# Performance work log

Hardware: AMD Instinct MI355X
Metric: run time of the kernel (lower is better)

The kernel has to match this reference:

```python
import jax, jax.numpy as jnp
import numpy as np
from jax import lax

B, L, D = 2, 2048, 2048
H, DK, DV, K = 16, 128, 128, 4
Q_DIM = H * DK  # 2048
V_DIM = H * DV  # 2048


def setup_inputs() -> dict:
    key = jax.random.key(0)
    ks = jax.random.split(key, 16)
    s = 0.02
    f32 = jnp.float32
    return {
        "hidden_states": jax.random.normal(ks[0], (B, L, D), f32),
        "Wq": jax.random.normal(ks[1], (D, Q_DIM), f32) * s,
        "Wk": jax.random.normal(ks[2], (D, Q_DIM), f32) * s,
        "Wv": jax.random.normal(ks[3], (D, V_DIM), f32) * s,
        "Wb": jax.random.normal(ks[4], (D, H), f32) * s,
        "bb": jnp.full((H,), -2.0, f32),  # beta_proj bias init -2.0
        "Wg": jax.random.normal(ks[5], (D, V_DIM), f32) * s,
        "Wo": jax.random.normal(ks[6], (V_DIM, D), f32) * s,
        "qconv_w": jax.random.normal(ks[7], (Q_DIM, K), f32) * 0.5,
        "qconv_b": jnp.zeros((Q_DIM,), f32),
        "kconv_w": jax.random.normal(ks[8], (Q_DIM, K), f32) * 0.5,
        "kconv_b": jnp.zeros((Q_DIM,), f32),
        "qn_w": jnp.ones((DK,), f32),
        "qn_b": jnp.zeros((DK,), f32),
        "kn_w": jnp.ones((DK,), f32),
        "kn_b": jnp.zeros((DK,), f32),
    }


def silu(x):
    return x * jax.nn.sigmoid(x)


def causal_dwconv(x, w, b):
    # x: (B,L,C), depthwise causal conv, w: (C,K), b: (C,)
    Kk = w.shape[1]
    xp = jnp.pad(x, ((0, 0), (Kk - 1, 0), (0, 0)))
    kern = w.T[:, None, :]  # (K, 1, C) for WIO depthwise
    y = lax.conv_general_dilated(
        xp, kern, window_strides=(1,), padding='VALID',
        dimension_numbers=('NWC', 'WIO', 'NWC'),
        feature_group_count=w.shape[0])
    return y + b


def layernorm(x, w, b, eps=1e-5):
    m = jnp.mean(x, axis=-1, keepdims=True)
    var = jnp.mean((x - m) ** 2, axis=-1, keepdims=True)
    return (x - m) * lax.rsqrt(var + eps) * w + b


def reference(hidden_states, Wq, Wk, Wv, Wb, bb, Wg, Wo,
              qconv_w, qconv_b, kconv_w, kconv_b, qn_w, qn_b, kn_w, kn_b):
    Bs, Ls, Ds = hidden_states.shape
    q = hidden_states @ Wq
    k = hidden_states @ Wk
    v = hidden_states @ Wv
    beta = jax.nn.sigmoid(hidden_states @ Wb + bb)        # (B,L,H)
    gate = silu(hidden_states @ Wg)                       # (B,L,V)
    q = silu(causal_dwconv(q, qconv_w, qconv_b))
    k = silu(causal_dwconv(k, kconv_w, kconv_b))
    q = layernorm(q.reshape(Bs, Ls, H, DK), qn_w, qn_b)
    k = layernorm(k.reshape(Bs, Ls, H, DK), kn_w, kn_b)
    v = v.reshape(Bs, Ls, H, DV)
    # time-major for scan: (L,B,H,*)
    qs = q.transpose(1, 0, 2, 3)
    ks_ = k.transpose(1, 0, 2, 3)
    vs = v.transpose(1, 0, 2, 3)
    bs = beta.transpose(1, 0, 2)                          # (L,B,H)
    S0 = jnp.zeros((Bs, H, DV, DK), hidden_states.dtype)

    def step(S, inp):
        q_t, k_t, v_t, b_t = inp
        b = b_t[..., None, None]                          # (B,H,1,1)
        S = (1.0 - b) * S + b * (v_t[..., :, None] * k_t[..., None, :])
        o_t = jnp.einsum('bhvk,bhk->bhv', S, q_t)
        return S, o_t

    _, os = lax.scan(step, S0, (qs, ks_, vs, bs))         # os: (L,B,H,DV)
    o = os.transpose(1, 0, 2, 3).reshape(Bs, Ls, H * DV)
    o = o * gate
    return o @ Wo
```

## Files before the change

kernel.cpp:

```cpp
#include <hip/hip_runtime.h>

#define DEV __device__ __forceinline__

typedef __attribute__((ext_vector_type(4))) float f32x4;
typedef __attribute__((ext_vector_type(8))) short s16x8;
typedef __attribute__((ext_vector_type(8))) unsigned short u16x8;
typedef __attribute__((ext_vector_type(4))) unsigned short u16x4;

DEV unsigned short f2bf(float f) {
    union { float f; unsigned u; } v; v.f = f;
    unsigned r = v.u + 0x7fffu + ((v.u >> 16) & 1u);
    return (unsigned short)(r >> 16);
}
DEV float bf2f(unsigned short b) {
    union { unsigned u; float f; } v; v.u = ((unsigned)b) << 16;
    return v.f;
}
DEV f32x4 mfma16(s16x8 a, s16x8 b, f32x4 c) {
    return __builtin_amdgcn_mfma_f32_16x16x32_bf16(a, b, c, 0, 0, 0);
}
DEV float sigmoidf_(float x) { return 1.f / (1.f + __expf(-x)); }

typedef __attribute__((address_space(3))) unsigned int lds_u32;
typedef const __attribute__((address_space(1))) unsigned int glob_u32;
DEV void gload16(const void* g, void* l) {
    __builtin_amdgcn_global_load_lds((glob_u32*)g, (lds_u32*)l, 16, 0, 0);
}

static constexpr int Bc = 2, Lc = 2048, Dc = 2048, Hc = 16, DKc = 128;

__global__ __launch_bounds__(256) void hsconv_kernel(const float* __restrict__ src,
                                                     unsigned short* __restrict__ dst) {
    size_t i8 = ((size_t)blockIdx.x * 256 + threadIdx.x) * 8;
    f32x4 a = *(const f32x4*)(src + i8);
    f32x4 b = *(const f32x4*)(src + i8 + 4);
    u16x8 r;
    for (int j = 0; j < 4; ++j) { r[j] = f2bf(a[j]); r[j + 4] = f2bf(b[j]); }
    *(u16x8*)(dst + i8) = r;
}

struct WcArgs { const float* src[5]; unsigned short* dst[5]; };

__global__ __launch_bounds__(256) void wconv_kernel(WcArgs wa) {
    __shared__ unsigned short t[64][66];
    const float* __restrict__ src = wa.src[blockIdx.z];
    unsigned short* __restrict__ dst = wa.dst[blockIdx.z];
    const int k0 = blockIdx.x * 64, n0 = blockIdx.y * 64;
    const int tid = threadIdx.x;
    for (int it = 0; it < 4; ++it) {
        int idx = it * 256 + tid;
        int k = idx >> 4, n = (idx & 15) * 4;
        f32x4 v = *(const f32x4*)(src + (size_t)(k0 + k) * 2048 + n0 + n);
        for (int j = 0; j < 4; ++j) t[k][n + j] = f2bf(v[j]);
    }
    __syncthreads();
    for (int it = 0; it < 4; ++it) {
        int idx = it * 256 + tid;
        int n = idx >> 4, k = (idx & 15) * 4;
        u16x4 o;
        for (int j = 0; j < 4; ++j) o[j] = t[k + j][n];
        *(u16x4*)(dst + (size_t)(n0 + n) * 2048 + k0 + k) = o;
    }
}

__global__ __launch_bounds__(256) void wbt_kernel(const float* __restrict__ Wb,
                                                  unsigned short* __restrict__ wbt) {
    int g = blockIdx.x * 256 + threadIdx.x;
    int n = g >> 8;
    int k0 = (g & 255) * 8;
    u16x8 r;
    for (int j = 0; j < 8; ++j) r[j] = f2bf(Wb[(size_t)(k0 + j) * 16 + n]);
    *(u16x8*)(wbt + (size_t)n * 2048 + k0) = r;
}

struct GpArgs { const unsigned short* B[4]; unsigned short* C[4]; };

#define GEMM_BODY(A_, Bt_, KDIM)                                                          \
    __shared__ unsigned short As[128 * 64];                                               \
    __shared__ unsigned short Bs[128 * 64];                                               \
    const int tid = threadIdx.x, lane = tid & 63, wid = tid >> 6;                         \
    const int l15 = lane & 15, lq = lane >> 4;                                            \
    const int wr = wid >> 1, wc = wid & 1;                                                \
    const int m0 = blockIdx.x * 128, n0 = blockIdx.y * 128;                               \
    const int rsub = lane >> 3, csub = (lane & 7) * 8;                                    \
    f32x4 acc[4][4] = {};                                                                 \
    for (int kt = 0; kt < KDIM; kt += 64) {                                               \
        for (int j = 0; j < 4; ++j) {                                                     \
            int seg = j * 4 + wid;                                                        \
            gload16(A_ + (size_t)(m0 + seg * 8 + rsub) * KDIM + kt + csub, &As[seg * 512]); \
            gload16(Bt_ + (size_t)(n0 + seg * 8 + rsub) * KDIM + kt + csub, &Bs[seg * 512]); \
        }                                                                                 \
        __syncthreads();                                                                  \
        for (int kh = 0; kh < 2; ++kh) {                                                  \
            s16x8 af[4];                                                                  \
            for (int m16 = 0; m16 < 4; ++m16)                                             \
                af[m16] = *(const s16x8*)&As[(wr * 64 + m16 * 16 + l15) * 64 + kh * 32 + 8 * lq]; \
            for (int n16 = 0; n16 < 4; ++n16) {                                           \
                s16x8 bf = *(const s16x8*)&Bs[(wc * 64 + n16 * 16 + l15) * 64 + kh * 32 + 8 * lq]; \
                for (int m16 = 0; m16 < 4; ++m16)                                         \
                    acc[m16][n16] = mfma16(af[m16], bf, acc[m16][n16]);                   \
            }                                                                             \
        }                                                                                 \
        __syncthreads();                                                                  \
    }

__global__ __launch_bounds__(256) void gemm_proj(const unsigned short* __restrict__ A,
                                                 GpArgs ga, int N, int K) {
    const unsigned short* __restrict__ Bt = ga.B[blockIdx.z];
    GEMM_BODY(A, Bt, K)
    unsigned short* __restrict__ C = ga.C[blockIdx.z];
    for (int m16 = 0; m16 < 4; ++m16)
        for (int n16 = 0; n16 < 4; ++n16) {
            int row = m0 + wr * 64 + m16 * 16 + 4 * lq;
            int col = n0 + wc * 64 + n16 * 16 + l15;
            for (int j = 0; j < 4; ++j)
                C[(size_t)(row + j) * N + col] = f2bf(acc[m16][n16][j]);
        }
}

__global__ __launch_bounds__(256) void gemm_out(const unsigned short* __restrict__ A,
                                                const unsigned short* __restrict__ Bt,
                                                float* __restrict__ C, int N, int K) {
    GEMM_BODY(A, Bt, K)
    for (int m16 = 0; m16 < 4; ++m16)
        for (int n16 = 0; n16 < 4; ++n16) {
            int row = m0 + wr * 64 + m16 * 16 + 4 * lq;
            int col = n0 + wc * 64 + n16 * 16 + l15;
            for (int j = 0; j < 4; ++j)
                C[(size_t)(row + j) * N + col] = acc[m16][n16][j];
        }
}

__global__ __launch_bounds__(256) void beta_kernel(const unsigned short* __restrict__ hsb,
                                                   const unsigned short* __restrict__ wbt,
                                                   const float* __restrict__ bb,
                                                   float* __restrict__ bbuf,
                                                   float* __restrict__ labuf) {
    const int tid = threadIdx.x, lane = tid & 63, wid = tid >> 6;
    const int l15 = lane & 15, lq = lane >> 4;
    const int row16 = blockIdx.x * 64 + wid * 16;
    f32x4 acc = {};
    for (int kt = 0; kt < 2048; kt += 32) {
        s16x8 a = *(const s16x8*)(hsb + (size_t)(row16 + l15) * 2048 + kt + 8 * lq);
        s16x8 b = *(const s16x8*)(wbt + (size_t)l15 * 2048 + kt + 8 * lq);
        acc = mfma16(a, b, acc);
    }
    float bias = bb[l15];
    for (int j = 0; j < 4; ++j) {
        int i = row16 + 4 * lq + j;
        float x = acc[j] + bias;
        bbuf[(size_t)i * 16 + l15] = sigmoidf_(x);
        labuf[(size_t)i * 16 + l15] = -(fmaxf(x, 0.f) + log1pf(__expf(-fabsf(x))));
    }
}

__global__ __launch_bounds__(256) void convln_kernel(const unsigned short* __restrict__ src,
                                                     const float* __restrict__ cw,
                                                     const float* __restrict__ cb,
                                                     const float* __restrict__ lw,
                                                     const float* __restrict__ lb,
                                                     unsigned short* __restrict__ dst) {
    const int bl = blockIdx.x;
    const int tid = threadIdx.x;
    const int b = bl >> 11, l = bl & 2047;
    const int c0 = tid * 8;
    const int ch0 = c0 & 127;
    f32x4 wv[8];
    for (int i = 0; i < 8; ++i) wv[i] = *(const f32x4*)(cw + (size_t)(c0 + i) * 4);
    float acc[8];
    {
        f32x4 ca = *(const f32x4*)(cb + c0);
        f32x4 cbv = *(const f32x4*)(cb + c0 + 4);
        for (int i = 0; i < 4; ++i) { acc[i] = ca[i]; acc[4 + i] = cbv[i]; }
    }
    for (int j = 0; j < 4; ++j) {
        int lj = l - 3 + j;
        if (lj < 0) continue;
        u16x8 v = *(const u16x8*)(src + ((size_t)(b * 2048 + lj)) * 2048 + c0);
        for (int i = 0; i < 8; ++i) acc[i] += wv[i][j] * bf2f(v[i]);
    }
    float y[8];
    float s1 = 0.f, s2 = 0.f;
    for (int i = 0; i < 8; ++i) {
        float t = acc[i];
        t = t * sigmoidf_(t);
        y[i] = t; s1 += t; s2 += t * t;
    }
    for (int o = 8; o; o >>= 1) { s1 += __shfl_xor(s1, o, 16); s2 += __shfl_xor(s2, o, 16); }
    float m = s1 * (1.f / 128.f);
    float var = s2 * (1.f / 128.f) - m * m;
    float r = rsqrtf(var + 1e-5f);
    f32x4 lwa = *(const f32x4*)(lw + ch0), lwb = *(const f32x4*)(lw + ch0 + 4);
    f32x4 lba = *(const f32x4*)(lb + ch0), lbb = *(const f32x4*)(lb + ch0 + 4);
    u16x8 outv;
    for (int i = 0; i < 4; ++i) {
        outv[i]     = f2bf((y[i]     - m) * r * lwa[i] + lba[i]);
        outv[4 + i] = f2bf((y[4 + i] - m) * r * lwb[i] + lbb[i]);
    }
    *(u16x8*)(dst + (size_t)bl * 2048 + c0) = outv;
}

__global__ __launch_bounds__(256) void recur_kernel(const unsigned short* __restrict__ qln,
                                                    const unsigned short* __restrict__ kln,
                                                    const unsigned short* __restrict__ vp,
                                                    const float* __restrict__ bbuf,
                                                    const float* __restrict__ labuf,
                                                    unsigned short* __restrict__ orec) {
    __shared__ unsigned short Qs[64][136];
    __shared__ unsigned short Ks[64][136];
    __shared__ unsigned short Kt[128][72];
    __shared__ unsigned short Vt[32][72];
    __shared__ unsigned short Ps[64][72];
    __shared__ unsigned short Simg[32][136];
    __shared__ float ls[64], es[64], wsc[64], bsc[64];
    __shared__ float gam;

    const int tid = threadIdx.x;
    const int lane = tid & 63, wid = tid >> 6;
    const int l15 = lane & 15, lq = lane >> 4;
    const int bh = blockIdx.x, vs = blockIdx.y;
    const int b = bh >> 4, h = bh & 15;
    const size_t rowBase = (size_t)b * 2048;
    const int voff = h * 128 + vs * 32;
    const int vt_own = wid & 1;
    const int ktb = (wid >> 1) * 4;

    f32x4 accS[4] = {};

    for (int ch = 0; ch < 32; ++ch) {
        const int t0 = ch * 64;
        if (wid == 0) {
            float la = labuf[(rowBase + t0 + lane) * 16 + h];
            float bv = bbuf[(rowBase + t0 + lane) * 16 + h];
            float l = la;
            for (int o = 1; o < 64; o <<= 1) { float n = __shfl_up(l, o, 64); if (lane >= o) l += n; }
            ls[lane] = l;
            es[lane] = __expf(l);
            float l63 = __shfl(l, 63, 64);
            wsc[lane] = __expf(l63 - l) * bv;
            bsc[lane] = bv;
            if (lane == 0) gam = __expf(l63);
            for (int it = 0; it < 16; ++it) {
                int idx = it * 64 + lane;
                int r = idx >> 4, c8 = (idx & 15) * 8;
                *(u16x8*)&Qs[r][c8] = *(const u16x8*)(qln + (rowBase + t0 + r) * 2048 + h * 128 + c8);
            }
        } else if (wid == 1) {
            for (int it = 0; it < 16; ++it) {
                int idx = it * 64 + lane;
                int r = idx >> 4, c8 = (idx & 15) * 8;
                *(u16x8*)&Ks[r][c8] = *(const u16x8*)(kln + (rowBase + t0 + r) * 2048 + h * 128 + c8);
            }
        } else if (wid == 2) {
            for (int c8 = 0; c8 < 128; c8 += 8) {
                u16x8 kv = *(const u16x8*)(kln + (rowBase + t0 + lane) * 2048 + h * 128 + c8);
                for (int ii = 0; ii < 8; ++ii) Kt[c8 + ii][lane] = kv[ii];
            }
        } else {
            for (int c8 = 0; c8 < 32; c8 += 8) {
                u16x8 vv = *(const u16x8*)(vp + (rowBase + t0 + lane) * 2048 + voff + c8);
                for (int ii = 0; ii < 8; ++ii) Vt[c8 + ii][lane] = vv[ii];
            }
        }
        __syncthreads();

        {
            const int i0 = wid * 16;
            f32x4 accp[4] = {};
            for (int kt = 0; kt < 4; ++kt) {
                s16x8 af = *(const s16x8*)&Qs[i0 + l15][kt * 32 + 8 * lq];
                for (int s16i = 0; s16i < 4; ++s16i) {
                    s16x8 bf = *(const s16x8*)&Ks[s16i * 16 + l15][kt * 32 + 8 * lq];
                    accp[s16i] = mfma16(af, bf, accp[s16i]);
                }
            }
            for (int s16i = 0; s16i < 4; ++s16i)
                for (int j = 0; j < 4; ++j) {
                    int i = i0 + 4 * lq + j;
                    int s = s16i * 16 + l15;
                    float pv = accp[s16i][j];
                    pv = (s <= i) ? pv * __expf(ls[i] - ls[s]) * bsc[s] : 0.f;
                    Ps[i][s] = f2bf(pv);
                }
            for (int q = 0; q < 4; ++q)
                for (int j = 0; j < 4; ++j) {
                    int v = vt_own * 16 + 4 * lq + j;
                    int k = (ktb + q) * 16 + l15;
                    Simg[v][k] = f2bf(accS[q][j]);
                }
        }
        __syncthreads();

        {
            const int i0 = wid * 16;
            f32x4 ae[2] = {}, ai[2] = {};
            for (int kt = 0; kt < 4; ++kt) {
                s16x8 af = *(const s16x8*)&Qs[i0 + l15][kt * 32 + 8 * lq];
                for (int vt = 0; vt < 2; ++vt) {
                    s16x8 bf = *(const s16x8*)&Simg[vt * 16 + l15][kt * 32 + 8 * lq];
                    ae[vt] = mfma16(af, bf, ae[vt]);
                }
            }
            for (int st = 0; st < 2; ++st) {
                s16x8 af = *(const s16x8*)&Ps[i0 + l15][st * 32 + 8 * lq];
                for (int vt = 0; vt < 2; ++vt) {
                    s16x8 bf = *(const s16x8*)&Vt[vt * 16 + l15][st * 32 + 8 * lq];
                    ai[vt] = mfma16(af, bf, ai[vt]);
                }
            }
            for (int vt = 0; vt < 2; ++vt)
                for (int j = 0; j < 4; ++j) {
                    int i = i0 + 4 * lq + j;
                    float o = es[i] * ae[vt][j] + ai[vt][j];
                    orec[(rowBase + t0 + i) * 2048 + voff + vt * 16 + l15] = f2bf(o);
                }
        }

        {
            float g = gam;
            for (int q = 0; q < 4; ++q)
                for (int j = 0; j < 4; ++j) accS[q][j] *= g;
            for (int st = 0; st < 2; ++st) {
                s16x8 vraw = *(const s16x8*)&Vt[vt_own * 16 + l15][st * 32 + 8 * lq];
                s16x8 aw;
                for (int ii = 0; ii < 8; ++ii) {
                    int s = st * 32 + 8 * lq + ii;
                    aw[ii] = (short)f2bf(bf2f((unsigned short)vraw[ii]) * wsc[s]);
                }
                for (int q = 0; q < 4; ++q) {
                    s16x8 bf = *(const s16x8*)&Kt[(ktb + q) * 16 + l15][st * 32 + 8 * lq];
                    accS[q] = mfma16(aw, bf, accS[q]);
                }
            }
        }
        __syncthreads();
    }
}

__global__ __launch_bounds__(256) void gate_kernel(const unsigned short* __restrict__ o,
                                                   unsigned short* __restrict__ g) {
    size_t i8 = ((size_t)blockIdx.x * 256 + threadIdx.x) * 8;
    u16x8 ov = *(const u16x8*)(o + i8);
    u16x8 gv = *(const u16x8*)(g + i8);
    u16x8 r;
    for (int ii = 0; ii < 8; ++ii) {
        float gf = bf2f(gv[ii]);
        r[ii] = f2bf(bf2f(ov[ii]) * gf * sigmoidf_(gf));
    }
    *(u16x8*)(g + i8) = r;
}

extern "C" void kernel_launch(void* const* d_in, const int* in_sizes, int n_in,
                              void* d_out, int out_size, void* d_ws, size_t ws_size,
                              hipStream_t stream) {
    const float* hs  = (const float*)d_in[0];
    const float* Wq  = (const float*)d_in[1];
    const float* Wk  = (const float*)d_in[2];
    const float* Wv  = (const float*)d_in[3];
    const float* Wb  = (const float*)d_in[4];
    const float* bbv = (const float*)d_in[5];
    const float* Wg  = (const float*)d_in[6];
    const float* Wo  = (const float*)d_in[7];
    const float* qcw = (const float*)d_in[8];
    const float* qcb = (const float*)d_in[9];
    const float* kcw = (const float*)d_in[10];
    const float* kcb = (const float*)d_in[11];
    const float* qnw = (const float*)d_in[12];
    const float* qnb = (const float*)d_in[13];
    const float* knw = (const float*)d_in[14];
    const float* knb = (const float*)d_in[15];
    float* out = (float*)d_out;

    char* ws = (char*)d_ws;
    const size_t S2 = (size_t)Bc * Lc * 2048 * 2;
    const size_t WSb = (size_t)2048 * 2048 * 2;
    const size_t BB = (size_t)Bc * Lc * Hc * 4;
    unsigned short* hsb  = (unsigned short*)(ws);
    unsigned short* wqt  = (unsigned short*)(ws + S2);
    unsigned short* wkt  = (unsigned short*)(ws + S2 + 1 * WSb);
    unsigned short* wvt  = (unsigned short*)(ws + S2 + 2 * WSb);
    unsigned short* wgt  = (unsigned short*)(ws + S2 + 3 * WSb);
    unsigned short* wot  = (unsigned short*)(ws + S2 + 4 * WSb);
    unsigned short* qp   = (unsigned short*)(ws + S2 + 5 * WSb);
    unsigned short* kp   = (unsigned short*)(ws + S2 + 5 * WSb + 1 * S2);
    unsigned short* vp   = (unsigned short*)(ws + S2 + 5 * WSb + 2 * S2);
    unsigned short* gp   = (unsigned short*)(ws + S2 + 5 * WSb + 3 * S2);
    float* bbuf  = (float*)(ws + S2 + 5 * WSb + 4 * S2);
    float* labuf = (float*)(ws + S2 + 5 * WSb + 4 * S2 + BB);
    unsigned short* wbt = (unsigned short*)(ws + S2 + 5 * WSb + 4 * S2 + 2 * BB);
    unsigned short* qln  = wqt;
    unsigned short* kln  = wvt;
    unsigned short* orec = qp;

    const int M = Bc * Lc;

    hsconv_kernel<<<dim3(M * 2048 / (256 * 8)), dim3(256), 0, stream>>>(hs, hsb);
    WcArgs wa;
    wa.src[0] = Wq; wa.src[1] = Wk; wa.src[2] = Wv; wa.src[3] = Wg; wa.src[4] = Wo;
    wa.dst[0] = wqt; wa.dst[1] = wkt; wa.dst[2] = wvt; wa.dst[3] = wgt; wa.dst[4] = wot;
    wconv_kernel<<<dim3(32, 32, 5), dim3(256), 0, stream>>>(wa);
    wbt_kernel<<<dim3(16), dim3(256), 0, stream>>>(Wb, wbt);

    GpArgs ga;
    ga.B[0] = wqt; ga.B[1] = wkt; ga.B[2] = wvt; ga.B[3] = wgt;
    ga.C[0] = qp;  ga.C[1] = kp;  ga.C[2] = vp;  ga.C[3] = gp;
    gemm_proj<<<dim3(M / 128, 2048 / 128, 4), dim3(256), 0, stream>>>(hsb, ga, 2048, 2048);

    beta_kernel<<<dim3(M / 64), dim3(256), 0, stream>>>(hsb, wbt, bbv, bbuf, labuf);
    convln_kernel<<<dim3(M), dim3(256), 0, stream>>>(qp, qcw, qcb, qnw, qnb, qln);
    convln_kernel<<<dim3(M), dim3(256), 0, stream>>>(kp, kcw, kcb, knw, knb, kln);
    recur_kernel<<<dim3(Bc * Hc, 4), dim3(256), 0, stream>>>(qln, kln, vp, bbuf, labuf, orec);
    gate_kernel<<<dim3(M * 2048 / 8 / 256), dim3(256), 0, stream>>>(orec, gp);
    gemm_out<<<dim3(M / 128, 2048 / 128, 1), dim3(256), 0, stream>>>(gp, wot, out, 2048, 2048);
}
```

Before: 572.5 us.

## Split chunked recurrence into parallel local, state-scan, and cross-chunk kernels

Replaces the sequential per-(b,h) chunk loop, which ran on only 128 blocks, with three kernels. The first computes intra-chunk outputs and per-chunk state deltas for all 32 chunks in parallel. The second runs a cheap elementwise scan of the chunk states with the decay factors. The third adds the inter-chunk contribution Q·S to the outputs. This exposes far more parallelism on a large GPU, at the cost of writing chunk states to global memory in bf16 (reusing the hsb/kp buffers), extra launches, and a read-modify-write of orec.

```diff
diff --git a/kernel.cpp b/kernel.cpp
--- a/kernel.cpp
+++ b/kernel.cpp
@@ -28,6 +28,12 @@
 }
 
 static constexpr int Bc = 2, Lc = 2048, Dc = 2048, Hc = 16, DKc = 128;
+static constexpr size_t SLOT = 524288;
+
+DEV unsigned short* dslot(unsigned short* d0, unsigned short* d1, int c, int bh) {
+    unsigned short* p = (c < 16) ? d0 + (size_t)c * SLOT : d1 + (size_t)(c - 16) * SLOT;
+    return p + (size_t)bh * 16384;
+}
 
 __global__ __launch_bounds__(256) void hsconv_kernel(const float* __restrict__ src,
                                                      unsigned short* __restrict__ dst) {
@@ -200,140 +206,196 @@
     *(u16x8*)(dst + (size_t)bl * 2048 + c0) = outv;
 }
 
-__global__ __launch_bounds__(256) void recur_kernel(const unsigned short* __restrict__ qln,
-                                                    const unsigned short* __restrict__ kln,
-                                                    const unsigned short* __restrict__ vp,
-                                                    const float* __restrict__ bbuf,
-                                                    const float* __restrict__ labuf,
-                                                    unsigned short* __restrict__ orec) {
+__global__ __launch_bounds__(256) void recur_local(const unsigned short* __restrict__ qln,
+                                                   const unsigned short* __restrict__ kln,
+                                                   const unsigned short* __restrict__ vp,
+                                                   const float* __restrict__ bbuf,
+                                                   const float* __restrict__ labuf,
+                                                   unsigned short* __restrict__ orec,
+                                                   unsigned short* __restrict__ d0,
+                                                   unsigned short* __restrict__ d1,
+                                                   float* __restrict__ es_buf,
+                                                   float* __restrict__ gamma_buf) {
     __shared__ unsigned short Qs[64][136];
     __shared__ unsigned short Ks[64][136];
     __shared__ unsigned short Kt[128][72];
-    __shared__ unsigned short Vt[32][72];
+    __shared__ unsigned short Vt[128][72];
     __shared__ unsigned short Ps[64][72];
-    __shared__ unsigned short Simg[32][136];
-    __shared__ float ls[64], es[64], wsc[64], bsc[64];
-    __shared__ float gam;
+    __shared__ float ls[64], wsc[64], bsc[64];
 
     const int tid = threadIdx.x;
     const int lane = tid & 63, wid = tid >> 6;
     const int l15 = lane & 15, lq = lane >> 4;
-    const int bh = blockIdx.x, vs = blockIdx.y;
+    const int bh = blockIdx.x, c = blockIdx.y;
     const int b = bh >> 4, h = bh & 15;
     const size_t rowBase = (size_t)b * 2048;
-    const int voff = h * 128 + vs * 32;
-    const int vt_own = wid & 1;
-    const int ktb = (wid >> 1) * 4;
-
-    f32x4 accS[4] = {};
-
-    for (int ch = 0; ch < 32; ++ch) {
-        const int t0 = ch * 64;
-        if (wid == 0) {
-            float la = labuf[(rowBase + t0 + lane) * 16 + h];
-            float bv = bbuf[(rowBase + t0 + lane) * 16 + h];
-            float l = la;
-            for (int o = 1; o < 64; o <<= 1) { float n = __shfl_up(l, o, 64); if (lane >= o) l += n; }
-            ls[lane] = l;
-            es[lane] = __expf(l);
-            float l63 = __shfl(l, 63, 64);
-            wsc[lane] = __expf(l63 - l) * bv;
-            bsc[lane] = bv;
-            if (lane == 0) gam = __expf(l63);
-            for (int it = 0; it < 16; ++it) {
-                int idx = it * 64 + lane;
-                int r = idx >> 4, c8 = (idx & 15) * 8;
-                *(u16x8*)&Qs[r][c8] = *(const u16x8*)(qln + (rowBase + t0 + r) * 2048 + h * 128 + c8);
+    const int t0 = c * 64;
+
+    if (wid == 0) {
+        float la = labuf[(rowBase + t0 + lane) * 16 + h];
+        float bv = bbuf[(rowBase + t0 + lane) * 16 + h];
+        float l = la;
+        for (int o = 1; o < 64; o <<= 1) { float n = __shfl_up(l, o, 64); if (lane >= o) l += n; }
+        ls[lane] = l;
+        es_buf[(size_t)bh * 2048 + t0 + lane] = __expf(l);
+        float l63 = __shfl(l, 63, 64);
+        wsc[lane] = __expf(l63 - l) * bv;
+        bsc[lane] = bv;
+        if (lane == 0) gamma_buf[bh * 32 + c] = __expf(l63);
+        for (int it = 0; it < 16; ++it) {
+            int idx = it * 64 + lane;
+            int r = idx >> 4, c8 = (idx & 15) * 8;
+            *(u16x8*)&Qs[r][c8] = *(const u16x8*)(qln + (rowBase + t0 + r) * 2048 + h * 128 + c8);
+        }
+    } else if (wid == 1) {
+        for (int it = 0; it < 16; ++it) {
+            int idx = it * 64 + lane;
+            int r = idx >> 4, c8 = (idx & 15) * 8;
+            *(u16x8*)&Ks[r][c8] = *(const u16x8*)(kln + (rowBase + t0 + r) * 2048 + h * 128 + c8);
+        }
+    } else if (wid == 2) {
+        for (int c8 = 0; c8 < 128; c8 += 8) {
+            u16x8 kv = *(const u16x8*)(kln + (rowBase + t0 + lane) * 2048 + h * 128 + c8);
+            for (int ii = 0; ii < 8; ++ii) Kt[c8 + ii][lane] = kv[ii];
+        }
+    } else {
+        for (int c8 = 0; c8 < 128; c8 += 8) {
+            u16x8 vv = *(const u16x8*)(vp + (rowBase + t0 + lane) * 2048 + h * 128 + c8);
+            for (int ii = 0; ii < 8; ++ii) Vt[c8 + ii][lane] = vv[ii];
+        }
+    }
+    __syncthreads();
+
+    const int i0 = wid * 16;
+    {
+        f32x4 accp[4] = {};
+        for (int kt = 0; kt < 4; ++kt) {
+            s16x8 af = *(const s16x8*)&Qs[i0 + l15][kt * 32 + 8 * lq];
+            for (int s16i = 0; s16i < 4; ++s16i) {
+                s16x8 bf = *(const s16x8*)&Ks[s16i * 16 + l15][kt * 32 + 8 * lq];
+                accp[s16i] = mfma16(af, bf, accp[s16i]);
             }
-        } else if (wid == 1) {
-            for (int it = 0; it < 16; ++it) {
-                int idx = it * 64 + lane;
-                int r = idx >> 4, c8 = (idx & 15) * 8;
-                *(u16x8*)&Ks[r][c8] = *(const u16x8*)(kln + (rowBase + t0 + r) * 2048 + h * 128 + c8);
+        }
+        for (int s16i = 0; s16i < 4; ++s16i)
+            for (int j = 0; j < 4; ++j) {
+                int i = i0 + 4 * lq + j;
+                int s = s16i * 16 + l15;
+                float pv = accp[s16i][j];
+                pv = (s <= i) ? pv * __expf(ls[i] - ls[s]) * bsc[s] : 0.f;
+                Ps[i][s] = f2bf(pv);
             }
-        } else if (wid == 2) {
-            for (int c8 = 0; c8 < 128; c8 += 8) {
-                u16x8 kv = *(const u16x8*)(kln + (rowBase + t0 + lane) * 2048 + h * 128 + c8);
-                for (int ii = 0; ii < 8; ++ii) Kt[c8 + ii][lane] = kv[ii];
+    }
+    __syncthreads();
+
+    {
+        f32x4 ai[8] = {};
+        for (int st = 0; st < 2; ++st) {
+            s16x8 af = *(const s16x8*)&Ps[i0 + l15][st * 32 + 8 * lq];
+            for (int vt = 0; vt < 8; ++vt) {
+                s16x8 bf = *(const s16x8*)&Vt[vt * 16 + l15][st * 32 + 8 * lq];
+                ai[vt] = mfma16(af, bf, ai[vt]);
             }
-        } else {
-            for (int c8 = 0; c8 < 32; c8 += 8) {
-                u16x8 vv = *(const u16x8*)(vp + (rowBase + t0 + lane) * 2048 + voff + c8);
-                for (int ii = 0; ii < 8; ++ii) Vt[c8 + ii][lane] = vv[ii];
+        }
+        for (int vt = 0; vt < 8; ++vt)
+            for (int j = 0; j < 4; ++j) {
+                int i = i0 + 4 * lq + j;
+                orec[(rowBase + t0 + i) * 2048 + h * 128 + vt * 16 + l15] = f2bf(ai[vt][j]);
             }
-        }
-        __syncthreads();
-
-        {
-            const int i0 = wid * 16;
-            f32x4 accp[4] = {};
-            for (int kt = 0; kt < 4; ++kt) {
-                s16x8 af = *(const s16x8*)&Qs[i0 + l15][kt * 32 + 8 * lq];
-                for (int s16i = 0; s16i < 4; ++s16i) {
-                    s16x8 bf = *(const s16x8*)&Ks[s16i * 16 + l15][kt * 32 + 8 * lq];
-                    accp[s16i] = mfma16(af, bf, accp[s16i]);
-                }
-            }
-            for (int s16i = 0; s16i < 4; ++s16i)
-                for (int j = 0; j < 4; ++j) {
-                    int i = i0 + 4 * lq + j;
-                    int s = s16i * 16 + l15;
-                    float pv = accp[s16i][j];
-                    pv = (s <= i) ? pv * __expf(ls[i] - ls[s]) * bsc[s] : 0.f;
-                    Ps[i][s] = f2bf(pv);
-                }
-            for (int q = 0; q < 4; ++q)
-                for (int j = 0; j < 4; ++j) {
-                    int v = vt_own * 16 + 4 * lq + j;
-                    int k = (ktb + q) * 16 + l15;
-                    Simg[v][k] = f2bf(accS[q][j]);
-                }
-        }
-        __syncthreads();
-
-        {
-            const int i0 = wid * 16;
-            f32x4 ae[2] = {}, ai[2] = {};
-            for (int kt = 0; kt < 4; ++kt) {
-                s16x8 af = *(const s16x8*)&Qs[i0 + l15][kt * 32 + 8 * lq];
-                for (int vt = 0; vt < 2; ++vt) {
-                    s16x8 bf = *(const s16x8*)&Simg[vt * 16 + l15][kt * 32 + 8 * lq];
-                    ae[vt] = mfma16(af, bf, ae[vt]);
-                }
-            }
-            for (int st = 0; st < 2; ++st) {
-                s16x8 af = *(const s16x8*)&Ps[i0 + l15][st * 32 + 8 * lq];
-                for (int vt = 0; vt < 2; ++vt) {
-                    s16x8 bf = *(const s16x8*)&Vt[vt * 16 + l15][st * 32 + 8 * lq];
-                    ai[vt] = mfma16(af, bf, ai[vt]);
-                }
-            }
-            for (int vt = 0; vt < 2; ++vt)
-                for (int j = 0; j < 4; ++j) {
-                    int i = i0 + 4 * lq + j;
-                    float o = es[i] * ae[vt][j] + ai[vt][j];
-                    orec[(rowBase + t0 + i) * 2048 + voff + vt * 16 + l15] = f2bf(o);
-                }
-        }
-
-        {
-            float g = gam;
-            for (int q = 0; q < 4; ++q)
-                for (int j = 0; j < 4; ++j) accS[q][j] *= g;
-            for (int st = 0; st < 2; ++st) {
-                s16x8 vraw = *(const s16x8*)&Vt[vt_own * 16 + l15][st * 32 + 8 * lq];
+    }
+
+    if (c < 31) {
+        f32x4 accD[2][8] = {};
+        for (int st = 0; st < 2; ++st) {
+            for (int vtl = 0; vtl < 2; ++vtl) {
+                s16x8 vraw = *(const s16x8*)&Vt[(wid * 2 + vtl) * 16 + l15][st * 32 + 8 * lq];
                 s16x8 aw;
                 for (int ii = 0; ii < 8; ++ii) {
                     int s = st * 32 + 8 * lq + ii;
                     aw[ii] = (short)f2bf(bf2f((unsigned short)vraw[ii]) * wsc[s]);
                 }
-                for (int q = 0; q < 4; ++q) {
-                    s16x8 bf = *(const s16x8*)&Kt[(ktb + q) * 16 + l15][st * 32 + 8 * lq];
-                    accS[q] = mfma16(aw, bf, accS[q]);
+                for (int q = 0; q < 8; ++q) {
+                    s16x8 bfk = *(const s16x8*)&Kt[q * 16 + l15][st * 32 + 8 * lq];
+                    accD[vtl][q] = mfma16(aw, bfk, accD[vtl][q]);
                 }
             }
         }
-        __syncthreads();
+        unsigned short* D = dslot(d0, d1, c, bh);
+        for (int vtl = 0; vtl < 2; ++vtl)
+            for (int q = 0; q < 8; ++q)
+                for (int j = 0; j < 4; ++j) {
+                    int v = wid * 32 + vtl * 16 + 4 * lq + j;
+                    int k = q * 16 + l15;
+                    D[v * 128 + k] = f2bf(accD[vtl][q][j]);
+                }
+    }
+}
+
+__global__ __launch_bounds__(256) void recur_scan(unsigned short* __restrict__ d0,
+                                                  unsigned short* __restrict__ d1,
+                                                  const float* __restrict__ gamma_buf) {
+    const int bid = blockIdx.x;
+    const int bh = bid >> 4, sl = bid & 15;
+    const int off = sl * 1024 + threadIdx.x * 4;
+    f32x4 running = {};
+    for (int c = 0; c < 32; ++c) {
+        u16x4 dv;
+        if (c < 31) dv = *(const u16x4*)(dslot(d0, d1, c, bh) + off);
+        if (c >= 1) {
+            u16x4 s;
+            for (int j = 0; j < 4; ++j) s[j] = f2bf(running[j]);
+            *(u16x4*)(dslot(d0, d1, c - 1, bh) + off) = s;
+        }
+        if (c < 31) {
+            float g = gamma_buf[bh * 32 + c];
+            for (int j = 0; j < 4; ++j) running[j] = g * running[j] + bf2f(dv[j]);
+        }
+    }
+}
+
+__global__ __launch_bounds__(256) void recur_cross(const unsigned short* __restrict__ qln,
+                                                   unsigned short* __restrict__ orec,
+                                                   unsigned short* __restrict__ d0,
+                                                   unsigned short* __restrict__ d1,
+                                                   const float* __restrict__ es_buf) {
+    __shared__ unsigned short Sl[128][136];
+    __shared__ unsigned short Qs[64][136];
+    const int tid = threadIdx.x;
+    const int lane = tid & 63, wid = tid >> 6;
+    const int l15 = lane & 15, lq = lane >> 4;
+    const int bh = blockIdx.x, c = blockIdx.y + 1;
+    const int b = bh >> 4, h = bh & 15;
+    const size_t rowBase = (size_t)b * 2048;
+    const int t0 = c * 64;
+
+    const unsigned short* S = dslot(d0, d1, c - 1, bh);
+    for (int it = 0; it < 8; ++it) {
+        int e = it * 2048 + tid * 8;
+        *(u16x8*)&Sl[e >> 7][e & 127] = *(const u16x8*)(S + e);
+    }
+    for (int it = 0; it < 4; ++it) {
+        int e = it * 2048 + tid * 8;
+        *(u16x8*)&Qs[e >> 7][e & 127] =
+            *(const u16x8*)(qln + (rowBase + t0 + (e >> 7)) * 2048 + h * 128 + (e & 127));
+    }
+    __syncthreads();
+
+    const int i0 = wid * 16;
+    f32x4 ae[8] = {};
+    for (int kt = 0; kt < 4; ++kt) {
+        s16x8 af = *(const s16x8*)&Qs[i0 + l15][kt * 32 + 8 * lq];
+        for (int vt = 0; vt < 8; ++vt) {
+            s16x8 bf = *(const s16x8*)&Sl[vt * 16 + l15][kt * 32 + 8 * lq];
+            ae[vt] = mfma16(af, bf, ae[vt]);
+        }
+    }
+    for (int j = 0; j < 4; ++j) {
+        int i = i0 + 4 * lq + j;
+        float e = es_buf[(size_t)bh * 2048 + t0 + i];
+        size_t base = (rowBase + t0 + i) * 2048 + h * 128;
+        for (int vt = 0; vt < 8; ++vt) {
+            size_t a = base + vt * 16 + l15;
+            orec[a] = f2bf(bf2f(orec[a]) + e * ae[vt][j]);
+        }
     }
 }
 
@@ -385,9 +447,12 @@
     unsigned short* kp   = (unsigned short*)(ws + S2 + 5 * WSb + 1 * S2);
     unsigned short* vp   = (unsigned short*)(ws + S2 + 5 * WSb + 2 * S2);
     unsigned short* gp   = (unsigned short*)(ws + S2 + 5 * WSb + 3 * S2);
-    float* bbuf  = (float*)(ws + S2 + 5 * WSb + 4 * S2);
-    float* labuf = (float*)(ws + S2 + 5 * WSb + 4 * S2 + BB);
-    unsigned short* wbt = (unsigned short*)(ws + S2 + 5 * WSb + 4 * S2 + 2 * BB);
+    char* tail = ws + S2 + 5 * WSb + 4 * S2;
+    float* bbuf  = (float*)(tail);
+    float* labuf = (float*)(tail + BB);
+    unsigned short* wbt = (unsigned short*)(tail + 2 * BB);
+    float* es_buf = (float*)(tail + 2 * BB + 65536);
+    float* gamma_buf = (float*)(tail + 2 * BB + 65536 + 262144);
     unsigned short* qln  = wqt;
     unsigned short* kln  = wvt;
     unsigned short* orec = qp;
@@ -409,7 +474,12 @@
     beta_kernel<<<dim3(M / 64), dim3(256), 0, stream>>>(hsb, wbt, bbv, bbuf, labuf);
     convln_kernel<<<dim3(M), dim3(256), 0, stream>>>(qp, qcw, qcb, qnw, qnb, qln);
     convln_kernel<<<dim3(M), dim3(256), 0, stream>>>(kp, kcw, kcb, knw, knb, kln);
-    recur_kernel<<<dim3(Bc * Hc, 4), dim3(256), 0, stream>>>(qln, kln, vp, bbuf, labuf, orec);
+
+    recur_local<<<dim3(Bc * Hc, 32), dim3(256), 0, stream>>>(qln, kln, vp, bbuf, labuf,
+                                                             orec, hsb, kp, es_buf, gamma_buf);
+    recur_scan<<<dim3(Bc * Hc * 16), dim3(256), 0, stream>>>(hsb, kp, gamma_buf);
+    recur_cross<<<dim3(Bc * Hc, 31), dim3(256), 0, stream>>>(qln, orec, hsb, kp, es_buf);
+
     gate_kernel<<<dim3(M * 2048 / 8 / 256), dim3(256), 0, stream>>>(orec, gp);
     gemm_out<<<dim3(M / 128, 2048 / 128, 1), dim3(256), 0, stream>>>(gp, wot, out, 2048, 2048);
 }
```

After: 512.3 us. 1.12x faster.
